# Kernel optimization log

Hardware: AMD Instinct MI355X
Metric: run time of the kernel (lower is better)

The kernel has to match this reference:

```python
import jax, jax.numpy as jnp
import numpy as np

EPS = 1e-5
BN_SCALE = 1.0 / np.sqrt(1.0 + EPS)  # inference BN with running_mean=0, running_var=1


def lrelu(x):
    return jnp.where(x >= 0, x, 0.2 * x)


def bn_affine(x, g, b, axis=1):
    shp = [1] * x.ndim
    shp[axis] = -1
    return x * (g.reshape(shp) * BN_SCALE) + b.reshape(shp)


def knn_idx(x, k):
    # x: (B, C, N) -> (B, N, k) indices of k nearest neighbors (incl. self)
    x2 = jnp.sum(x * x, axis=1)                       # (B, N)
    inner = jnp.einsum('bcn,bcm->bnm', x, x)          # (B, N, N)
    neg_dist = 2.0 * inner - x2[:, :, None] - x2[:, None, :]
    return jax.lax.top_k(neg_dist, k)[1]


def graph_feature(x, k):
    # x: (B, C, N) -> (B, 2C, N, k) edge features [x_j - x_i, x_i]
    B, C, N = x.shape
    idx = knn_idx(x, k)                               # (B, N, k)
    xt = jnp.transpose(x, (0, 2, 1))                  # (B, N, C)
    nbr = xt[jnp.arange(B)[:, None, None], idx]       # (B, N, k, C)
    ctr = xt[:, :, None, :]                           # (B, N, 1, C)
    feat = jnp.concatenate([nbr - ctr, jnp.broadcast_to(ctr, nbr.shape)], axis=-1)
    return jnp.transpose(feat, (0, 3, 1, 2))          # (B, 2C, N, k)


def edge_conv(x, W, g, b, k):
    # get_graph_feature -> 1x1 conv -> BN -> LeakyReLU -> max over neighbors
    f = graph_feature(x, k)
    h = jnp.einsum('oc,bcnk->bonk', W, f)
    return jnp.max(lrelu(bn_affine(h, g, b, axis=1)), axis=-1)  # (B, O, N)


def fps(xyz, m):
    # xyz: (B, 3, N) -> (B, m) farthest-point-sample indices, starting at index 0
    B, _, N = xyz.shape
    pts = jnp.transpose(xyz, (0, 2, 1))               # (B, N, 3)

    def body(carry, _):
        dists, last = carry
        p = jnp.take_along_axis(pts, last[:, None, None], axis=1)  # (B, 1, 3)
        d = jnp.sum((pts - p) ** 2, axis=-1)          # (B, N)
        dists = jnp.minimum(dists, d)
        nxt = jnp.argmax(dists, axis=-1).astype(jnp.int32)
        return (dists, nxt), last

    init = (jnp.full((B, N), 1e10, dtype=xyz.dtype), jnp.zeros((B,), jnp.int32))
    _, idxs = jax.lax.scan(body, init, None, length=m)
    return jnp.transpose(idxs, (1, 0))                # (B, m)


def gather_ch(x, idx):
    # x: (B, C, N), idx: (B, M) -> (B, C, M)
    B, C, _ = x.shape
    return jnp.take_along_axis(x, jnp.broadcast_to(idx[:, None, :], (B, C, idx.shape[1])), axis=2)


def aggregate(xyz, node, features, k):
    # xyz: (B,3,N), node: (B,3,M), features: (B,C,N) -> (B,C,M)
    B = xyz.shape[0]
    x2 = jnp.sum(xyz * xyz, axis=1)                   # (B, N)
    n2 = jnp.sum(node * node, axis=1)                 # (B, M)
    inner = jnp.einsum('bcm,bcn->bmn', node, xyz)     # (B, M, N)
    neg_d = 2.0 * inner - n2[:, :, None] - x2[:, None, :]
    idx = jax.lax.top_k(neg_d, k)[1]                  # (B, M, k) nearest points per node
    ft = jnp.transpose(features, (0, 2, 1))           # (B, N, C)
    grp = ft[jnp.arange(B)[:, None, None], idx]       # (B, M, k, C)
    return jnp.transpose(jnp.max(grp, axis=2), (0, 2, 1))  # (B, C, M)


def setup_inputs() -> dict:
    key = jax.random.key(0)
    ks = jax.random.split(key, 32)
    B, N, K, E = 8, 2048, 20, 1024

    def w(k_, o, c):
        return jax.random.normal(k_, (o, c), jnp.float32) / np.sqrt(c)

    def gb(k_, c):
        k1, k2 = jax.random.split(k_)
        return (jax.random.uniform(k1, (c,), jnp.float32, 0.5, 1.5),
                0.1 * jax.random.normal(k2, (c,), jnp.float32))

    g1, b1 = gb(ks[1], 64); g2, b2 = gb(ks[2], 64); g2m, b2m = gb(ks[3], E)
    g3, b3 = gb(ks[4], 256); g4, b4 = gb(ks[5], 256); g5, b5 = gb(ks[6], E)
    g6, b6 = gb(ks[7], 512); g7, b7 = gb(ks[8], 256)
    return {
        'x': jax.random.normal(ks[0], (B, 3, N), jnp.float32),
        'W1': w(ks[10], 64, 6), 'g1': g1, 'b1': b1,
        'W2': w(ks[11], 64, 128), 'g2': g2, 'b2': b2,
        'W2m': w(ks[12], E, 128), 'g2m': g2m, 'b2m': b2m,
        'W3': w(ks[13], 256, 512), 'g3': g3, 'b3': b3,
        'W4': w(ks[14], 256, 512), 'g4': g4, 'b4': b4,
        'W5': w(ks[15], E, 512), 'g5': g5, 'b5': b5,
        'Wl1': w(ks[16], 512, 2 * E), 'g6': g6, 'b6': b6,
        'Wl2': w(ks[17], 256, 512), 'bl2': 0.01 * jax.random.normal(ks[18], (256,), jnp.float32),
        'g7': g7, 'b7': b7,
        'Wl3': w(ks[19], 40, 256), 'bl3': 0.01 * jax.random.normal(ks[20], (40,), jnp.float32),
    }


def reference(x, W1, g1, b1, W2, g2, b2, W2m, g2m, b2m, W3, g3, b3,
              W4, g4, b4, W5, g5, b5, Wl1, g6, b6, Wl2, bl2, g7, b7, Wl3, bl3):
    K = 20
    B, _, N = x.shape
    xyz = x

    x1 = edge_conv(x, W1, g1, b1, K)                  # (B, 64, N)
    x2 = edge_conv(x1, W2, g2, b2, K)                 # (B, 64, N)
    xt1_ = jnp.concatenate([x1, x2], axis=1)          # (B, 128, N)
    xt1 = lrelu(bn_affine(jnp.einsum('oc,bcn->bon', W2m, xt1_), g2m, b2m, axis=1))

    idx = fps(xyz, N // 4)                            # (B, N/4)
    node1 = gather_ch(xyz, idx)                       # (B, 3, N/4)
    nf1 = gather_ch(xt1_, idx)                        # (B, 128, N/4)
    agg = aggregate(xyz, node1, xt1_, K)              # (B, 128, N/4)
    xm = jnp.concatenate([nf1, agg], axis=1)          # (B, 256, N/4)

    x3 = edge_conv(xm, W3, g3, b3, K // 2)            # (B, 256, N/4)
    x4 = edge_conv(x3, W4, g4, b4, K // 2)            # (B, 256, N/4)
    xt2 = lrelu(bn_affine(jnp.einsum('oc,bcn->bon', W5, jnp.concatenate([x3, x4], axis=1)), g5, b5, axis=1))

    v = jnp.concatenate([jnp.max(xt1, axis=-1), jnp.max(xt2, axis=-1)], axis=1)  # (B, 2E)
    h = lrelu(bn_affine(v @ Wl1.T, g6, b6, axis=1))   # dropout = identity (eval)
    h = lrelu(bn_affine(h @ Wl2.T + bl2, g7, b7, axis=1))
    logits = h @ Wl3.T + bl3                          # (B, 40)
    return (logits, node1)
```

## Files before the change

### kernel.cpp

```cpp
#include <hip/hip_runtime.h>

#define BN_SCALE 0.9999950000374997f

template <int CTRL>
__device__ __forceinline__ float dpp_fmax_step(float v) {
  int xi = __builtin_bit_cast(int, v);
  int ti = __builtin_amdgcn_update_dpp(xi, xi, CTRL, 0xf, 0xf, false);
  return fmaxf(v, __builtin_bit_cast(float, ti));
}
template <int CTRL>
__device__ __forceinline__ int dpp_imin_step(int v) {
  int t = __builtin_amdgcn_update_dpp(v, v, CTRL, 0xf, 0xf, false);
  return (t < v) ? t : v;
}
template <int CTRL>
__device__ __forceinline__ float dpp_fadd_step(float v) {
  int ti = __builtin_amdgcn_update_dpp(0, __builtin_bit_cast(int, v), CTRL, 0xf, 0xf, true);
  return v + __builtin_bit_cast(float, ti);
}
__device__ __forceinline__ float wave_fmax(float v) {
  v = dpp_fmax_step<0x111>(v);
  v = dpp_fmax_step<0x112>(v);
  v = dpp_fmax_step<0x114>(v);
  v = dpp_fmax_step<0x118>(v);
  v = dpp_fmax_step<0x142>(v);
  v = dpp_fmax_step<0x143>(v);
  return __builtin_bit_cast(float, __builtin_amdgcn_readlane(__builtin_bit_cast(int, v), 63));
}
__device__ __forceinline__ int wave_imin(int v) {
  v = dpp_imin_step<0x111>(v);
  v = dpp_imin_step<0x112>(v);
  v = dpp_imin_step<0x114>(v);
  v = dpp_imin_step<0x118>(v);
  v = dpp_imin_step<0x142>(v);
  v = dpp_imin_step<0x143>(v);
  return __builtin_amdgcn_readlane(v, 63);
}
__device__ __forceinline__ float wave_fadd(float v) {
  v = dpp_fadd_step<0x111>(v);
  v = dpp_fadd_step<0x112>(v);
  v = dpp_fadd_step<0x114>(v);
  v = dpp_fadd_step<0x118>(v);
  v = dpp_fadd_step<0x142>(v);
  v = dpp_fadd_step<0x143>(v);
  return __builtin_bit_cast(float, __builtin_amdgcn_readlane(__builtin_bit_cast(int, v), 63));
}

template <int R, bool SQPRE>
__device__ __forceinline__ void knn4_body(const float* __restrict__ Q, int qStrideB,
                                          const float* __restrict__ Xc, int cStrideB,
                                          int C, int M, int N, int k, int* __restrict__ idxOut,
                                          const float* __restrict__ sqPre,
                                          int b, int q0, char* smem) {
  constexpr int NR = 4 * R;
  float (*negd)[R * 256] = (float (*)[R * 256])smem;
  int tid = threadIdx.x;
  const float* qb = Q + (long)b * qStrideB + q0;
  const float* cb = Xc + (long)b * cStrideB;
  if constexpr (R % 4 == 0) {
    constexpr int H = R / 4;
    float d0[R], d1[R], d2[R], d3[R], sq[R];
    #pragma unroll
    for (int i = 0; i < R; ++i) { d0[i] = d1[i] = d2[i] = d3[i] = sq[i] = 0.f; }
    for (int c = 0; c < C; ++c) {
      float4 q4 = *(const float4*)(qb + (long)c * M);
      const float4* pc4 = (const float4*)(cb + (long)c * N);
      #pragma unroll
      for (int h = 0; h < H; ++h) {
        float4 xv = pc4[tid + 256 * h];
        if (!SQPRE) {
          sq[4 * h + 0] = fmaf(xv.x, xv.x, sq[4 * h + 0]);
          sq[4 * h + 1] = fmaf(xv.y, xv.y, sq[4 * h + 1]);
          sq[4 * h + 2] = fmaf(xv.z, xv.z, sq[4 * h + 2]);
          sq[4 * h + 3] = fmaf(xv.w, xv.w, sq[4 * h + 3]);
        }
        d0[4 * h + 0] = fmaf(q4.x, xv.x, d0[4 * h + 0]);
        d0[4 * h + 1] = fmaf(q4.x, xv.y, d0[4 * h + 1]);
        d0[4 * h + 2] = fmaf(q4.x, xv.z, d0[4 * h + 2]);
        d0[4 * h + 3] = fmaf(q4.x, xv.w, d0[4 * h + 3]);
        d1[4 * h + 0] = fmaf(q4.y, xv.x, d1[4 * h + 0]);
        d1[4 * h + 1] = fmaf(q4.y, xv.y, d1[4 * h + 1]);
        d1[4 * h + 2] = fmaf(q4.y, xv.z, d1[4 * h + 2]);
        d1[4 * h + 3] = fmaf(q4.y, xv.w, d1[4 * h + 3]);
        d2[4 * h + 0] = fmaf(q4.z, xv.x, d2[4 * h + 0]);
        d2[4 * h + 1] = fmaf(q4.z, xv.y, d2[4 * h + 1]);
        d2[4 * h + 2] = fmaf(q4.z, xv.z, d2[4 * h + 2]);
        d2[4 * h + 3] = fmaf(q4.z, xv.w, d2[4 * h + 3]);
        d3[4 * h + 0] = fmaf(q4.w, xv.x, d3[4 * h + 0]);
        d3[4 * h + 1] = fmaf(q4.w, xv.y, d3[4 * h + 1]);
        d3[4 * h + 2] = fmaf(q4.w, xv.z, d3[4 * h + 2]);
        d3[4 * h + 3] = fmaf(q4.w, xv.w, d3[4 * h + 3]);
      }
    }
    #pragma unroll
    for (int h = 0; h < H; ++h) {
      float4 s4;
      if (SQPRE) {
        s4 = ((const float4*)(sqPre + (long)b * N))[tid + 256 * h];
      } else {
        s4 = make_float4(sq[4 * h], sq[4 * h + 1], sq[4 * h + 2], sq[4 * h + 3]);
      }
      ((float4*)negd[0])[tid + 256 * h] =
          make_float4(2.f * d0[4 * h] - s4.x, 2.f * d0[4 * h + 1] - s4.y,
                      2.f * d0[4 * h + 2] - s4.z, 2.f * d0[4 * h + 3] - s4.w);
      ((float4*)negd[1])[tid + 256 * h] =
          make_float4(2.f * d1[4 * h] - s4.x, 2.f * d1[4 * h + 1] - s4.y,
                      2.f * d1[4 * h + 2] - s4.z, 2.f * d1[4 * h + 3] - s4.w);
      ((float4*)negd[2])[tid + 256 * h] =
          make_float4(2.f * d2[4 * h] - s4.x, 2.f * d2[4 * h + 1] - s4.y,
                      2.f * d2[4 * h + 2] - s4.z, 2.f * d2[4 * h + 3] - s4.w);
      ((float4*)negd[3])[tid + 256 * h] =
          make_float4(2.f * d3[4 * h] - s4.x, 2.f * d3[4 * h + 1] - s4.y,
                      2.f * d3[4 * h + 2] - s4.z, 2.f * d3[4 * h + 3] - s4.w);
    }
  } else {
    float d0[R], d1[R], d2[R], d3[R], sq[R];
    #pragma unroll
    for (int i = 0; i < R; ++i) { d0[i] = d1[i] = d2[i] = d3[i] = sq[i] = 0.f; }
    for (int c = 0; c < C; ++c) {
      float4 q4 = *(const float4*)(qb + (long)c * M);
      const float* pc = cb + (long)c * N;
      #pragma unroll
      for (int i = 0; i < R; ++i) {
        float xv = pc[tid + 256 * i];
        sq[i] = fmaf(xv, xv, sq[i]);
        d0[i] = fmaf(q4.x, xv, d0[i]);
        d1[i] = fmaf(q4.y, xv, d1[i]);
        d2[i] = fmaf(q4.z, xv, d2[i]);
        d3[i] = fmaf(q4.w, xv, d3[i]);
      }
    }
    #pragma unroll
    for (int i = 0; i < R; ++i) {
      int m = tid + 256 * i;
      negd[0][m] = 2.f * d0[i] - sq[i];
      negd[1][m] = 2.f * d1[i] - sq[i];
      negd[2][m] = 2.f * d2[i] - sq[i];
      negd[3][m] = 2.f * d3[i] - sq[i];
    }
  }
  __syncthreads();
  int lane = tid & 63, w = tid >> 6;
  const float* row = negd[w];
  int* outp = idxOut + ((long)b * M + (q0 + w)) * k;
  float v[NR];
  #pragma unroll
  for (int i = 0; i < NR; ++i) v[i] = row[lane + 64 * i];
  constexpr int G = NR / 4;
  for (int kk = 0; kk < k; ++kk) {
    float bv[G]; int br[G];
    #pragma unroll
    for (int g = 0; g < G; ++g) {
      float v0 = v[4 * g]; int r0 = 4 * g;
      #pragma unroll
      for (int j = 1; j < 4; ++j) {
        bool c = v[4 * g + j] > v0;
        v0 = c ? v[4 * g + j] : v0;
        r0 = c ? (4 * g + j) : r0;
      }
      bv[g] = v0; br[g] = r0;
    }
    #pragma unroll
    for (int s = G >> 1; s >= 1; s >>= 1) {
      #pragma unroll
      for (int i = 0; i < s; ++i) {
        bool c = bv[2 * i] >= bv[2 * i + 1];
        bv[i] = c ? bv[2 * i] : bv[2 * i + 1];
        br[i] = c ? br[2 * i] : br[2 * i + 1];
      }
    }
    float best = bv[0]; int ib = br[0];
    int bi = (best > -INFINITY) ? (lane + (ib << 6)) : N;
    float gmax = wave_fmax(best);
    int cand = (best == gmax) ? bi : 0x7FFFFFFF;
    int big = wave_imin(cand);
    if (lane == 0) outp[kk] = big;
    int ri = big >> 6;
    bool mine = (lane == (big & 63));
    #pragma unroll
    for (int i = 0; i < NR; ++i)
      if (i == ri) v[i] = mine ? -INFINITY : v[i];
  }
}

template <int R>
__global__ void knn4_kernel(const float* __restrict__ Q, int qStrideB,
                            const float* __restrict__ Xc, int cStrideB,
                            int C, int M, int N, int k, int* __restrict__ idxOut) {
  __shared__ __align__(16) char smem[R * 256 * 4 * 4];
  knn4_body<R, false>(Q, qStrideB, Xc, cStrideB, C, M, N, k, idxOut, nullptr,
                      blockIdx.y, blockIdx.x * 4, smem);
}

__device__ __forceinline__ void gemmPS_body(const float* __restrict__ X, int xStrideB, int C, int Np,
                                            const float* __restrict__ W, int ldw, int O,
                                            float* __restrict__ PtT, float* __restrict__ StT,
                                            int b, int n0, int o0, char* smem) {
  float (*Wp)[68] = (float (*)[68])smem;
  float (*Ws)[68] = (float (*)[68])(smem + 4352);
  float (*Xt)[68] = (float (*)[68])(smem + 8704);
  int tid = threadIdx.x;
  int to = tid % 16, tn = tid / 16;
  float accP[4][4] = {}, accS[4][4] = {};
  for (int c0 = 0; c0 < C; c0 += 16) {
    for (int e = tid; e < 16 * 64; e += 256) {
      int oo = e / 16, kk = e % 16;
      int c = c0 + kk, o = o0 + oo;
      bool ok = (c < C && o < O);
      Wp[kk][oo] = ok ? W[(long)o * ldw + c] : 0.f;
      Ws[kk][oo] = ok ? W[(long)o * ldw + C + c] : 0.f;
    }
    for (int e = tid; e < 16 * 64; e += 256) {
      int kk = e / 64, nn = e % 64;
      int c = c0 + kk, n = n0 + nn;
      Xt[kk][nn] = (c < C && n < Np) ? X[(long)b * xStrideB + (long)c * Np + n] : 0.f;
    }
    __syncthreads();
    for (int kk = 0; kk < 16; ++kk) {
      float4 xv = *(const float4*)&Xt[kk][tn * 4];
      float4 wp = *(const float4*)&Wp[kk][to * 4];
      float4 ws = *(const float4*)&Ws[kk][to * 4];
      float xs[4] = {xv.x, xv.y, xv.z, xv.w};
      float wps[4] = {wp.x, wp.y, wp.z, wp.w};
      float wss[4] = {ws.x, ws.y, ws.z, ws.w};
      #pragma unroll
      for (int i = 0; i < 4; ++i)
        #pragma unroll
        for (int j = 0; j < 4; ++j) {
          accP[i][j] = fmaf(xs[i], wps[j], accP[i][j]);
          accS[i][j] = fmaf(xs[i], wss[j], accS[i][j]);
        }
    }
    __syncthreads();
  }
  #pragma unroll
  for (int i = 0; i < 4; ++i) {
    int n = n0 + tn * 4 + i;
    if (n >= Np) continue;
    int o = o0 + to * 4;
    if (o + 3 < O) {
      long off = ((long)b * Np + n) * O + o;
      *(float4*)&PtT[off] = make_float4(accP[i][0], accP[i][1], accP[i][2], accP[i][3]);
      *(float4*)&StT[off] = make_float4(accS[i][0], accS[i][1], accS[i][2], accS[i][3]);
    } else {
      for (int j = 0; j < 4; ++j) {
        int oo = o + j;
        if (oo < O) {
          long off = ((long)b * Np + n) * O + oo;
          PtT[off] = accP[i][j];
          StT[off] = accS[i][j];
        }
      }
    }
  }
}

__device__ __forceinline__ void ecfinish_body64(const float* __restrict__ Pt, const float* __restrict__ St,
                                                const int* __restrict__ idx, int k, int O, int Np,
                                                const float* __restrict__ g, const float* __restrict__ bb,
                                                float* __restrict__ outp, long oStrideB,
                                                float* __restrict__ sqOut,
                                                int b, int blk) {
  int tid = threadIdx.x;
  int o = tid & 63;
  int n = blk * 4 + (tid >> 6);
  const float* PtB = Pt + (long)b * Np * O;
  const float* StB = St + (long)b * Np * O;
  const int* ip = idx + ((long)b * Np + n) * k;
  float mx = -INFINITY, mn = INFINITY;
  for (int kk = 0; kk < k; ++kk) {
    float v = PtB[(long)ip[kk] * O + o];
    mx = fmaxf(mx, v); mn = fminf(mn, v);
  }
  float ctrP = PtB[(long)n * O + o];
  float ctrS = StB[(long)n * O + o];
  float gs = g[o] * BN_SCALE;
  float m = (gs >= 0.f) ? mx : mn;
  float h = (ctrS - ctrP + m) * gs + bb[o];
  float out = h >= 0.f ? h : 0.2f * h;
  outp[(long)b * oStrideB + (long)o * Np + n] = out;
  if (sqOut) {
    int obits = __builtin_bit_cast(int, out);
    float acc = 0.f;
    #pragma unroll
    for (int c = 0; c < 64; ++c) {
      float hv = __builtin_bit_cast(float, __builtin_amdgcn_readlane(obits, c));
      acc = fmaf(hv, hv, acc);
    }
    if (o == 0) sqOut[(long)b * Np + n] = acc;
  }
}

__global__ void ecfinish_kernel(const float* __restrict__ Pt, const float* __restrict__ St,
                                const int* __restrict__ idx, int k, int O, int Np,
                                const float* __restrict__ g, const float* __restrict__ bb,
                                float* __restrict__ outp, long oStrideB) {
  int b = blockIdx.y;
  int n = blockIdx.x * blockDim.y + threadIdx.y;
  int o = threadIdx.x;
  const float* PtB = Pt + (long)b * Np * O;
  const float* StB = St + (long)b * Np * O;
  const int* ip = idx + ((long)b * Np + n) * k;
  float mx = -INFINITY, mn = INFINITY;
  for (int kk = 0; kk < k; ++kk) {
    float v = PtB[(long)ip[kk] * O + o];
    mx = fmaxf(mx, v); mn = fminf(mn, v);
  }
  float ctrP = PtB[(long)n * O + o];
  float ctrS = StB[(long)n * O + o];
  float gs = g[o] * BN_SCALE;
  float m = (gs >= 0.f) ? mx : mn;
  float h = (ctrS - ctrP + m) * gs + bb[o];
  outp[(long)b * oStrideB + (long)o * Np + n] = h >= 0.f ? h : 0.2f * h;
}

__device__ __forceinline__ void gemm_colmax_body(const float* __restrict__ X, int xStrideB, int C, int Np,
                                                 const float* __restrict__ W, int ldw, int O,
                                                 const float* __restrict__ g, const float* __restrict__ bb,
                                                 float* __restrict__ partial,
                                                 int b, int n0, int o0, int nt, int nNT, char* smem) {
  float (*Wt)[68] = (float (*)[68])smem;
  float (*Xt)[68] = (float (*)[68])(smem + 4352);
  int tid = threadIdx.x;
  int to = tid % 16, tn = tid / 16;
  float acc[4][4] = {};
  for (int c0 = 0; c0 < C; c0 += 16) {
    for (int e = tid; e < 16 * 64; e += 256) {
      int oo = e / 16, kk = e % 16;
      int c = c0 + kk, o = o0 + oo;
      Wt[kk][oo] = (c < C && o < O) ? W[(long)o * ldw + c] : 0.f;
    }
    for (int e = tid; e < 16 * 64; e += 256) {
      int kk = e / 64, nn = e % 64;
      int c = c0 + kk, n = n0 + nn;
      Xt[kk][nn] = (c < C && n < Np) ? X[(long)b * xStrideB + (long)c * Np + n] : 0.f;
    }
    __syncthreads();
    for (int kk = 0; kk < 16; ++kk) {
      float4 xv = *(const float4*)&Xt[kk][tn * 4];
      float4 wv = *(const float4*)&Wt[kk][to * 4];
      float xs[4] = {xv.x, xv.y, xv.z, xv.w};
      float wvs[4] = {wv.x, wv.y, wv.z, wv.w};
      #pragma unroll
      for (int i = 0; i < 4; ++i)
        #pragma unroll
        for (int j = 0; j < 4; ++j) acc[i][j] = fmaf(xs[i], wvs[j], acc[i][j]);
    }
    __syncthreads();
  }
  float vm[4];
  #pragma unroll
  for (int j = 0; j < 4; ++j) {
    int o = o0 + to * 4 + j;
    float gs = g[o] * BN_SCALE, bo = bb[o];
    float m = -INFINITY;
    #pragma unroll
    for (int i = 0; i < 4; ++i) {
      float h = acc[i][j] * gs + bo;
      h = h >= 0.f ? h : 0.2f * h;
      m = fmaxf(m, h);
    }
    vm[j] = m;
  }
  #pragma unroll
  for (int j = 0; j < 4; ++j) Xt[tn][to * 4 + j] = vm[j];
  __syncthreads();
  for (int s = 8; s > 0; s >>= 1) {
    if (tn < s)
      for (int j = 0; j < 4; ++j)
        Xt[tn][to * 4 + j] = fmaxf(Xt[tn][to * 4 + j], Xt[tn + s][to * 4 + j]);
    __syncthreads();
  }
  if (tn == 0)
    for (int j = 0; j < 4; ++j) {
      int o = o0 + to * 4 + j;
      partial[((long)b * nNT + nt) * O + o] = Xt[0][to * 4 + j];
    }
}

__global__ void gemm_colmax_kernel(const float* __restrict__ X, int xStrideB, int C, int Np,
                                   const float* __restrict__ W, int ldw, int O,
                                   const float* __restrict__ g, const float* __restrict__ bb,
                                   float* __restrict__ partial) {
  __shared__ __align__(16) char smem[8704];
  gemm_colmax_body(X, xStrideB, C, Np, W, ldw, O, g, bb, partial,
                   blockIdx.z, blockIdx.x * 64, blockIdx.y * 64, blockIdx.x, gridDim.x, smem);
}

__device__ __forceinline__ void xmfill_body(const float* __restrict__ xt1, int N,
                                            const int* __restrict__ fpsI,
                                            const int* __restrict__ idxA, int k, int M,
                                            float* __restrict__ xm, int xe) {
  long t = (long)xe * 256 + threadIdx.x;
  int i = (int)(t % M);
  int c = (int)((t / M) % 128);
  int b = (int)(t / ((long)128 * M));
  const float* xb = xt1 + (long)b * 128 * N + (long)c * N;
  float* xmB = xm + (long)b * 256 * M;
  xmB[(long)c * M + i] = xb[fpsI[(long)b * M + i]];
  const int* ip = idxA + ((long)b * M + i) * k;
  float best = -INFINITY;
  for (int kk = 0; kk < k; ++kk) best = fmaxf(best, xb[ip[kk]]);
  xmB[(long)(128 + c) * M + i] = best;
}

template <int FIRST, int LAST>
__device__ __forceinline__ void fps_body_rg(const float* __restrict__ xyz, int N, int M,
                                            int it0, int it1,
                                            int* __restrict__ fpsIdx, float* __restrict__ node1,
                                            float* __restrict__ distSv, int* __restrict__ lastSv,
                                            int b, char* smem) {
  #pragma clang fp contract(off)
  float4* sp4 = (float4*)smem;
  int*    fidx = (int*)(smem + 32768);
  float4* wvc  = (float4*)(smem + 32768 + 2048);
  int*    wis  = (int*)(smem + 32768 + 2048 + 128);
  int tid = threadIdx.x;
  int lane = tid & 63, w = tid >> 6;
  const float* xb = xyz + (long)b * 3 * N;
  for (int n = tid; n < N; n += 256) {
    sp4[((n & 7) << 8) | (n >> 3)] = make_float4(xb[n], xb[N + n], xb[2 * N + n], 0.f);
  }
  if (!FIRST) {
    for (int e = tid; e < it0; e += 256) fidx[e] = fpsIdx[(long)b * M + e];
  }
  __syncthreads();
  float4 pt[8];
  #pragma unroll
  for (int i = 0; i < 8; ++i) pt[i] = sp4[(i << 8) | tid];
  float dist[8];
  int last;
  float lx, ly, lz;
  if (FIRST) {
    #pragma unroll
    for (int i = 0; i < 8; ++i) dist[i] = 1e10f;
    last = 0;
    float4 l0 = sp4[0];
    lx = l0.x; ly = l0.y; lz = l0.z;
  } else {
    #pragma unroll
    for (int i = 0; i < 8; ++i) dist[i] = distSv[(long)b * 2048 + i * 256 + tid];
    last = lastSv[b];
    float4 lp = sp4[((last & 7) << 8) | (last >> 3)];
    lx = lp.x; ly = lp.y; lz = lp.z;
  }
  int base = tid * 8;
  for (int it = it0; it < it1; ++it) {
    int p = it & 1;
    if (tid == 0) fidx[it] = last;
    float best = -INFINITY; int bi = N;
    #pragma unroll
    for (int i = 0; i < 8; ++i) {
      float dx = pt[i].x - lx, dy = pt[i].y - ly, dz = pt[i].z - lz;
      float dx2 = dx * dx, dy2 = dy * dy, dz2 = dz * dz;
      float d = (dx2 + dy2) + dz2;
      float dn = dist[i];
      if (d < dn) dn = d;
      dist[i] = dn;
      if (dn > best) { best = dn; bi = base + i; }
    }
    float cx = pt[0].x, cy = pt[0].y, cz = pt[0].z;
    #pragma unroll
    for (int i = 1; i < 8; ++i) {
      bool c = (bi == base + i);
      cx = c ? pt[i].x : cx; cy = c ? pt[i].y : cy; cz = c ? pt[i].z : cz;
    }
    float gmax = wave_fmax(best);
    int cand = (best == gmax) ? bi : 0x7FFFFFFF;
    int wbi = wave_imin(cand);
    if (bi == wbi) { wvc[p * 4 + w] = make_float4(gmax, cx, cy, cz); wis[p * 4 + w] = wbi; }
    __syncthreads();
    float4 c0 = wvc[p * 4 + 0], c1 = wvc[p * 4 + 1], c2 = wvc[p * 4 + 2], c3 = wvc[p * 4 + 3];
    int i0 = wis[p * 4 + 0], i1 = wis[p * 4 + 1], i2 = wis[p * 4 + 2], i3 = wis[p * 4 + 3];
    float bv = c0.x; int bbi = i0; lx = c0.y; ly = c0.z; lz = c0.w;
    { bool c = (c1.x > bv) || (c1.x == bv && i1 < bbi);
      bv = c ? c1.x : bv; bbi = c ? i1 : bbi; lx = c ? c1.y : lx; ly = c ? c1.z : ly; lz = c ? c1.w : lz; }
    { bool c = (c2.x > bv) || (c2.x == bv && i2 < bbi);
      bv = c ? c2.x : bv; bbi = c ? i2 : bbi; lx = c ? c2.y : lx; ly = c ? c2.z : ly; lz = c ? c2.w : lz; }
    { bool c = (c3.x > bv) || (c3.x == bv && i3 < bbi);
      bv = c ? c3.x : bv; bbi = c ? i3 : bbi; lx = c ? c3.y : lx; ly = c ? c3.z : ly; lz = c ? c3.w : lz; }
    last = bbi;
  }
  if (!LAST) {
    for (int e = tid; e < it1; e += 256) {
      if (e >= it0) fpsIdx[(long)b * M + e] = fidx[e];
    }
    #pragma unroll
    for (int i = 0; i < 8; ++i) distSv[(long)b * 2048 + i * 256 + tid] = dist[i];
    if (tid == 0) lastSv[b] = last;
  } else {
    for (int e = tid; e < M; e += 256) fpsIdx[(long)b * M + e] = fidx[e];
    for (int e = tid; e < 3 * M; e += 256) {
      int c = e / M, i = e % M;
      int src = fidx[i];
      float4 ptc = sp4[((src & 7) << 8) | (src >> 3)];
      node1[(long)b * 3 * M + e] = (c == 0) ? ptc.x : (c == 1) ? ptc.y : ptc.z;
    }
  }
}

template <int FIRST, int LAST, bool SQP>
__global__ void knnfpsgemm_kernel(const float* __restrict__ Q, int qStrideB,
                                  const float* __restrict__ Xc, int cStrideB,
                                  int C, int Mq, int N, int k, int* __restrict__ idxOut,
                                  const float* __restrict__ W, int ldw, int O,
                                  float* __restrict__ Pt, float* __restrict__ St,
                                  const float* __restrict__ xyz, int Mf, int it0, int it1,
                                  int* __restrict__ fpsIdx, float* __restrict__ node1,
                                  float* __restrict__ distSv, int* __restrict__ lastSv,
                                  const float* __restrict__ sqPre,
                                  int nQblk, int nGblk, int nB) {
  __shared__ __align__(16) char smem[32768 + 2048 + 128 + 32];
  int bid = blockIdx.x;
  if (bid < nB) {
    __builtin_amdgcn_s_setprio(1);
    fps_body_rg<FIRST, LAST>(xyz, N, Mf, it0, it1, fpsIdx, node1, distSv, lastSv, bid, smem);
    __builtin_amdgcn_s_setprio(0);
  } else if (bid < nB + nB * nQblk) {
    int e = bid - nB;
    knn4_body<8, SQP>(Q, qStrideB, Xc, cStrideB, C, Mq, N, k, idxOut, sqPre,
                      e / nQblk, (e % nQblk) * 4, smem);
  } else {
    int e = bid - nB - nB * nQblk;
    gemmPS_body(Xc, cStrideB, C, N, W, ldw, O, Pt, St,
                e / nGblk, (e % nGblk) * 64, 0, smem);
  }
}

__global__ void ecfps_kernel(const float* __restrict__ Pt, const float* __restrict__ St,
                             const int* __restrict__ idx, int k, int O, int Np,
                             const float* __restrict__ g, const float* __restrict__ bb,
                             float* __restrict__ outp, long oStrideB,
                             float* __restrict__ sqOut,
                             const float* __restrict__ xyz, int N, int Mf, int it0, int it1,
                             int* __restrict__ fpsIdx, float* __restrict__ node1,
                             float* __restrict__ distSv, int* __restrict__ lastSv,
                             int nEperB, int nB) {
  __shared__ __align__(16) char smem[32768 + 2048 + 128 + 32];
  int bid = blockIdx.x;
  if (bid < nB) {
    __builtin_amdgcn_s_setprio(1);
    fps_body_rg<0, 0>(xyz, N, Mf, it0, it1, fpsIdx, node1, distSv, lastSv, bid, smem);
    __builtin_amdgcn_s_setprio(0);
  } else {
    int e = bid - nB;
    ecfinish_body64(Pt, St, idx, k, O, Np, g, bb, outp, oStrideB, sqOut,
                    e / nEperB, e % nEperB);
  }
}

__global__ void ecfagg_kernel(const float* __restrict__ Pt, const float* __restrict__ St,
                              const int* __restrict__ idxS2, int k2, int O2, int Np2,
                              const float* __restrict__ g2, const float* __restrict__ b2,
                              float* __restrict__ out2, long oStrideB2,
                              const float* __restrict__ Qn, int qStrideB,
                              const float* __restrict__ Xc, int cStrideB,
                              int Cq, int Mq, int Nc, int kq, int* __restrict__ idxAgg,
                              int nQblk, int nEperB) {
  __shared__ __align__(16) char smem[32768];
  int bid = blockIdx.x;
  if (bid % 5 == 0) {
    int a = bid / 5;
    knn4_body<8, false>(Qn, qStrideB, Xc, cStrideB, Cq, Mq, Nc, kq, idxAgg, nullptr,
                        a / nQblk, (a % nQblk) * 4, smem);
  } else {
    int e = bid - bid / 5 - 1;
    ecfinish_body64(Pt, St, idxS2, k2, O2, Np2, g2, b2, out2, oStrideB2, nullptr,
                    e / nEperB, e % nEperB);
  }
}

__global__ void colmaxxm_kernel(const float* __restrict__ X, int xStrideB, int C, int Np,
                                const float* __restrict__ W, int ldw, int O,
                                const float* __restrict__ g, const float* __restrict__ bb,
                                float* __restrict__ partial, int nNT, int nOT,
                                const float* __restrict__ xt1, int N,
                                const int* __restrict__ fpsI, const int* __restrict__ idxA,
                                int kq, int M, float* __restrict__ xm) {
  __shared__ __align__(16) char smem[8704];
  int bid = blockIdx.x;
  if (bid % 3 == 0) {
    xmfill_body(xt1, N, fpsI, idxA, kq, M, xm, bid / 3);
  } else {
    int e = bid - bid / 3 - 1;
    int per = nNT * nOT;
    int b = e / per, r = e % per;
    int nt = r % nNT, ot = r / nNT;
    gemm_colmax_body(X, xStrideB, C, Np, W, ldw, O, g, bb, partial,
                     b, nt * 64, ot * 64, nt, nNT, smem);
  }
}

__global__ void knngemm_kernel(const float* __restrict__ Xin, int xStrideB,
                               int C, int Mq, int N, int k, int* __restrict__ idxOut,
                               const float* __restrict__ W, int ldw, int O,
                               float* __restrict__ Pt, float* __restrict__ St,
                               int nQblk, int nGn, int nGo, int nB) {
  __shared__ __align__(16) char smem[13056];
  int bid = blockIdx.x;
  if (bid < nB * nQblk) {
    knn4_body<2, false>(Xin, xStrideB, Xin, xStrideB, C, Mq, N, k, idxOut, nullptr,
                        bid / nQblk, (bid % nQblk) * 4, smem);
  } else {
    int e = bid - nB * nQblk;
    int per = nGn * nGo;
    int b = e / per, r = e % per;
    int nt = r % nGn, ot = r / nGn;
    gemmPS_body(Xin, xStrideB, C, N, W, ldw, O, Pt, St, b, nt * 64, ot * 64, smem);
  }
}

__global__ void head_kernel(const float* __restrict__ partA, int NTa,
                            const float* __restrict__ partB, int NTb,
                            const float* __restrict__ Wl1, const float* __restrict__ g6, const float* __restrict__ b6,
                            const float* __restrict__ Wl2, const float* __restrict__ bl2,
                            const float* __restrict__ g7, const float* __restrict__ b7,
                            const float* __restrict__ Wl3, const float* __restrict__ bl3,
                            float* __restrict__ logits) {
  __shared__ float v[2048];
  __shared__ float h1[512];
  __shared__ float h2[256];
  int b = blockIdx.x, tid = threadIdx.x;
  int lane = tid & 63, w = tid >> 6;
  for (int o = tid; o < 1024; o += 256) {
    float m = -INFINITY;
    for (int t = 0; t < NTa; ++t) m = fmaxf(m, partA[((long)b * NTa + t) * 1024 + o]);
    v[o] = m;
    float m2 = -INFINITY;
    for (int t = 0; t < NTb; ++t) m2 = fmaxf(m2, partB[((long)b * NTb + t) * 1024 + o]);
    v[1024 + o] = m2;
  }
  __syncthreads();
  for (int o = w; o < 512; o += 4) {
    const float4* wr = (const float4*)(Wl1 + (long)o * 2048);
    const float4* vp = (const float4*)v;
    float s = 0.f;
    #pragma unroll
    for (int j = 0; j < 8; ++j) {
      float4 w4 = wr[lane + 64 * j];
      float4 v4 = vp[lane + 64 * j];
      s = fmaf(w4.x, v4.x, s); s = fmaf(w4.y, v4.y, s);
      s = fmaf(w4.z, v4.z, s); s = fmaf(w4.w, v4.w, s);
    }
    float t = wave_fadd(s);
    if (lane == 0) {
      float h = t * (g6[o] * BN_SCALE) + b6[o];
      h1[o] = h >= 0.f ? h : 0.2f * h;
    }
  }
  __syncthreads();
  for (int o = w; o < 256; o += 4) {
    const float4* wr = (const float4*)(Wl2 + (long)o * 512);
    const float4* hp = (const float4*)h1;
    float s = 0.f;
    #pragma unroll
    for (int j = 0; j < 2; ++j) {
      float4 w4 = wr[lane + 64 * j];
      float4 v4 = hp[lane + 64 * j];
      s = fmaf(w4.x, v4.x, s); s = fmaf(w4.y, v4.y, s);
      s = fmaf(w4.z, v4.z, s); s = fmaf(w4.w, v4.w, s);
    }
    float t = wave_fadd(s);
    if (lane == 0) {
      float sb = t + bl2[o];
      float h = sb * (g7[o] * BN_SCALE) + b7[o];
      h2[o] = h >= 0.f ? h : 0.2f * h;
    }
  }
  __syncthreads();
  for (int o = w; o < 40; o += 4) {
    const float4* wr = (const float4*)(Wl3 + (long)o * 256);
    const float4* hp = (const float4*)h2;
    float4 w4 = wr[lane];
    float4 v4 = hp[lane];
    float s = fmaf(w4.x, v4.x, 0.f);
    s = fmaf(w4.y, v4.y, s); s = fmaf(w4.z, v4.z, s); s = fmaf(w4.w, v4.w, s);
    float t = wave_fadd(s);
    if (lane == 0) logits[(long)b * 40 + o] = t + bl3[o];
  }
}

extern "C" void kernel_launch(void* const* d_in, const int* in_sizes, int n_in,
                              void* d_out, int out_size, void* d_ws, size_t ws_size,
                              hipStream_t stream) {
  const float* x   = (const float*)d_in[0];
  const float* W1  = (const float*)d_in[1];
  const float* g1  = (const float*)d_in[2];
  const float* b1  = (const float*)d_in[3];
  const float* W2  = (const float*)d_in[4];
  const float* g2  = (const float*)d_in[5];
  const float* b2  = (const float*)d_in[6];
  const float* W2m = (const float*)d_in[7];
  const float* g2m = (const float*)d_in[8];
  const float* b2m = (const float*)d_in[9];
  const float* W3  = (const float*)d_in[10];
  const float* g3  = (const float*)d_in[11];
  const float* b3  = (const float*)d_in[12];
  const float* W4  = (const float*)d_in[13];
  const float* g4  = (const float*)d_in[14];
  const float* b4  = (const float*)d_in[15];
  const float* W5  = (const float*)d_in[16];
  const float* g5  = (const float*)d_in[17];
  const float* b5  = (const float*)d_in[18];
  const float* Wl1 = (const float*)d_in[19];
  const float* g6  = (const float*)d_in[20];
  const float* b6  = (const float*)d_in[21];
  const float* Wl2 = (const float*)d_in[22];
  const float* bl2 = (const float*)d_in[23];
  const float* g7  = (const float*)d_in[24];
  const float* b7  = (const float*)d_in[25];
  const float* Wl3 = (const float*)d_in[26];
  const float* bl3 = (const float*)d_in[27];
  float* outF = (float*)d_out;

  const int B = 8, N = 2048, K = 20, M = 512, K2 = 10;

  float* ws    = (float*)d_ws;
  float* xt1   = ws;
  float* xm    = xt1 + (size_t)B * 128 * N;
  float* xc    = xm  + (size_t)B * 256 * M;
  float* Pt    = xc  + (size_t)B * 512 * M;
  float* St    = Pt  + (size_t)B * N * 64;
  float* partA = St  + (size_t)B * N * 64;
  float* partB = partA + (size_t)B * 32 * 1024;
  int*   idxK  = (int*)(partB + (size_t)B * 8 * 1024);
  int*   fpsI  = idxK + (size_t)B * N * K;
  float* fpsDist = (float*)(fpsI + (size_t)B * M);
  int*   fpsLast = (int*)(fpsDist + (size_t)B * 2048);
  int*   idxAgg  = fpsLast + 64;
  float* sqS2    = (float*)(idxAgg + (size_t)B * M * K);

  float* logits = outF;
  float* node1  = outF + 320;

  dim3 t256(256);
  const int nQblk = N / 4;
  const int nGblk = N / 64;
  const int nFused = B + B * nQblk + B * nGblk;
  const int nQa = M / 4;
  const int IT1 = 208, IT2 = 304;

  knnfpsgemm_kernel<1, 0, false><<<dim3(nFused), t256, 0, stream>>>(
      x, 3 * N, x, 3 * N, 3, N, N, K, idxK,
      W1, 6, 64, Pt, St,
      x, M, 0, IT1, fpsI, node1, fpsDist, fpsLast, nullptr, nQblk, nGblk, B);

  ecfps_kernel<<<dim3(B + B * (N / 4)), t256, 0, stream>>>(
      Pt, St, idxK, K, 64, N, g1, b1, xt1, (long)128 * N, sqS2,
      x, N, M, IT1, IT2, fpsI, node1, fpsDist, fpsLast, N / 4, B);

  knnfpsgemm_kernel<0, 1, true><<<dim3(nFused), t256, 0, stream>>>(
      xt1, 128 * N, xt1, 128 * N, 64, N, N, K, idxK,
      W2, 128, 64, Pt, St,
      x, M, IT2, M, fpsI, node1, fpsDist, fpsLast, sqS2, nQblk, nGblk, B);

  ecfagg_kernel<<<dim3(B * nQa + B * (N / 4)), t256, 0, stream>>>(
      Pt, St, idxK, K, 64, N, g2, b2, xt1 + (size_t)64 * N, (long)128 * N,
      node1, 3 * M, x, 3 * N, 3, M, N, K, idxAgg, nQa, N / 4);

  colmaxxm_kernel<<<dim3((B * 128 * M) / 256 + B * 32 * 16), t256, 0, stream>>>(
      xt1, 128 * N, 128, N, W2m, 128, 1024, g2m, b2m, partA, 32, 16,
      xt1, N, fpsI, idxAgg, K, M, xm);

  knngemm_kernel<<<dim3(B * nQa + B * (M / 64) * (256 / 64)), t256, 0, stream>>>(
      xm, 256 * M, 256, M, M, K2, idxK, W3, 512, 256, Pt, St, nQa, M / 64, 256 / 64, B);
  ecfinish_kernel<<<dim3(M, B), dim3(256, 1), 0, stream>>>(Pt, St, idxK, K2, 256, M, g3, b3, xc, (long)512 * M);

  knngemm_kernel<<<dim3(B * nQa + B * (M / 64) * (256 / 64)), t256, 0, stream>>>(
      xc, 512 * M, 256, M, M, K2, idxK, W4, 512, 256, Pt, St, nQa, M / 64, 256 / 64, B);
  ecfinish_kernel<<<dim3(M, B), dim3(256, 1), 0, stream>>>(Pt, St, idxK, K2, 256, M, g4, b4,
                                                           xc + (size_t)256 * M, (long)512 * M);

  gemm_colmax_kernel<<<dim3(M / 64, 1024 / 64, B), t256, 0, stream>>>(xc, 512 * M, 512, M, W5, 512, 1024,
                                                                      g5, b5, partB);

  head_kernel<<<dim3(B), t256, 0, stream>>>(partA, N / 64, partB, M / 64,
                                            Wl1, g6, b6, Wl2, bl2, g7, b7, Wl3, bl3, logits);
}
```

Measured before the change: 1.064 ms.

## Cache per-group maxima in knn top-k and split FPS points into SoA

The top-k selection in the knn body now keeps the per-group maxima of four values across iterations. After each pick it recomputes only the group that lost an element, instead of rescanning every value each round, which cuts the ALU work per selected neighbor. The FPS body stores point coordinates as three separate float arrays instead of padded float4. This shrinks shared memory so the fused kernels declare smaller LDS allocations, which may raise occupancy. The dynamic group recompute adds predicated branches over all groups, and the register layout changes.

```diff
diff --git a/kernel.cpp b/kernel.cpp
--- a/kernel.cpp
+++ b/kernel.cpp
@@ -147,29 +147,32 @@
   #pragma unroll
   for (int i = 0; i < NR; ++i) v[i] = row[lane + 64 * i];
   constexpr int G = NR / 4;
+  float bv[G]; int br[G];
+  #pragma unroll
+  for (int g = 0; g < G; ++g) {
+    float v0 = v[4 * g]; int r0 = 4 * g;
+    #pragma unroll
+    for (int j = 1; j < 4; ++j) {
+      bool c = v[4 * g + j] > v0;
+      v0 = c ? v[4 * g + j] : v0;
+      r0 = c ? (4 * g + j) : r0;
+    }
+    bv[g] = v0; br[g] = r0;
+  }
   for (int kk = 0; kk < k; ++kk) {
-    float bv[G]; int br[G];
-    #pragma unroll
-    for (int g = 0; g < G; ++g) {
-      float v0 = v[4 * g]; int r0 = 4 * g;
-      #pragma unroll
-      for (int j = 1; j < 4; ++j) {
-        bool c = v[4 * g + j] > v0;
-        v0 = c ? v[4 * g + j] : v0;
-        r0 = c ? (4 * g + j) : r0;
-      }
-      bv[g] = v0; br[g] = r0;
-    }
+    float mv[G]; int mi[G];
+    #pragma unroll
+    for (int g = 0; g < G; ++g) { mv[g] = bv[g]; mi[g] = br[g]; }
     #pragma unroll
     for (int s = G >> 1; s >= 1; s >>= 1) {
       #pragma unroll
       for (int i = 0; i < s; ++i) {
-        bool c = bv[2 * i] >= bv[2 * i + 1];
-        bv[i] = c ? bv[2 * i] : bv[2 * i + 1];
-        br[i] = c ? br[2 * i] : br[2 * i + 1];
+        bool c = mv[2 * i] >= mv[2 * i + 1];
+        mv[i] = c ? mv[2 * i] : mv[2 * i + 1];
+        mi[i] = c ? mi[2 * i] : mi[2 * i + 1];
       }
     }
-    float best = bv[0]; int ib = br[0];
+    float best = mv[0]; int ib = mi[0];
     int bi = (best > -INFINITY) ? (lane + (ib << 6)) : N;
     float gmax = wave_fmax(best);
     int cand = (best == gmax) ? bi : 0x7FFFFFFF;
@@ -180,6 +183,20 @@
     #pragma unroll
     for (int i = 0; i < NR; ++i)
       if (i == ri) v[i] = mine ? -INFINITY : v[i];
+    int gi = ri >> 2;
+    #pragma unroll
+    for (int g = 0; g < G; ++g) {
+      if (g == gi) {
+        float v0 = v[4 * g]; int r0 = 4 * g;
+        #pragma unroll
+        for (int j = 1; j < 4; ++j) {
+          bool c = v[4 * g + j] > v0;
+          v0 = c ? v[4 * g + j] : v0;
+          r0 = c ? (4 * g + j) : r0;
+        }
+        bv[g] = v0; br[g] = r0;
+      }
+    }
   }
 }
 
@@ -411,23 +428,29 @@
                                             float* __restrict__ distSv, int* __restrict__ lastSv,
                                             int b, char* smem) {
   #pragma clang fp contract(off)
-  float4* sp4 = (float4*)smem;
-  int*    fidx = (int*)(smem + 32768);
-  float4* wvc  = (float4*)(smem + 32768 + 2048);
-  int*    wis  = (int*)(smem + 32768 + 2048 + 128);
+  float* px = (float*)smem;
+  float* py = (float*)(smem + 8192);
+  float* pz = (float*)(smem + 16384);
+  int*   fidx = (int*)(smem + 24576);
+  float4* wvc = (float4*)(smem + 26624);
+  int*   wis  = (int*)(smem + 26752);
   int tid = threadIdx.x;
   int lane = tid & 63, w = tid >> 6;
   const float* xb = xyz + (long)b * 3 * N;
   for (int n = tid; n < N; n += 256) {
-    sp4[((n & 7) << 8) | (n >> 3)] = make_float4(xb[n], xb[N + n], xb[2 * N + n], 0.f);
+    int s = ((n & 7) << 8) | (n >> 3);
+    px[s] = xb[n]; py[s] = xb[N + n]; pz[s] = xb[2 * N + n];
   }
   if (!FIRST) {
     for (int e = tid; e < it0; e += 256) fidx[e] = fpsIdx[(long)b * M + e];
   }
   __syncthreads();
-  float4 pt[8];
+  float ptx[8], pty[8], ptz[8];
   #pragma unroll
-  for (int i = 0; i < 8; ++i) pt[i] = sp4[(i << 8) | tid];
+  for (int i = 0; i < 8; ++i) {
+    int s = (i << 8) | tid;
+    ptx[i] = px[s]; pty[i] = py[s]; ptz[i] = pz[s];
+  }
   float dist[8];
   int last;
   float lx, ly, lz;
@@ -435,14 +458,14 @@
     #pragma unroll
     for (int i = 0; i < 8; ++i) dist[i] = 1e10f;
     last = 0;
-    float4 l0 = sp4[0];
-    lx = l0.x; ly = l0.y; lz = l0.z;
+    int s0 = 0;
+    lx = px[s0]; ly = py[s0]; lz = pz[s0];
   } else {
     #pragma unroll
     for (int i = 0; i < 8; ++i) dist[i] = distSv[(long)b * 2048 + i * 256 + tid];
     last = lastSv[b];
-    float4 lp = sp4[((last & 7) << 8) | (last >> 3)];
-    lx = lp.x; ly = lp.y; lz = lp.z;
+    int sl = ((last & 7) << 8) | (last >> 3);
+    lx = px[sl]; ly = py[sl]; lz = pz[sl];
   }
   int base = tid * 8;
   for (int it = it0; it < it1; ++it) {
@@ -451,7 +474,7 @@
     float best = -INFINITY; int bi = N;
     #pragma unroll
     for (int i = 0; i < 8; ++i) {
-      float dx = pt[i].x - lx, dy = pt[i].y - ly, dz = pt[i].z - lz;
+      float dx = ptx[i] - lx, dy = pty[i] - ly, dz = ptz[i] - lz;
       float dx2 = dx * dx, dy2 = dy * dy, dz2 = dz * dz;
       float d = (dx2 + dy2) + dz2;
       float dn = dist[i];
@@ -459,11 +482,11 @@
       dist[i] = dn;
       if (dn > best) { best = dn; bi = base + i; }
     }
-    float cx = pt[0].x, cy = pt[0].y, cz = pt[0].z;
+    float cx = ptx[0], cy = pty[0], cz = ptz[0];
     #pragma unroll
     for (int i = 1; i < 8; ++i) {
       bool c = (bi == base + i);
-      cx = c ? pt[i].x : cx; cy = c ? pt[i].y : cy; cz = c ? pt[i].z : cz;
+      cx = c ? ptx[i] : cx; cy = c ? pty[i] : cy; cz = c ? ptz[i] : cz;
     }
     float gmax = wave_fmax(best);
     int cand = (best == gmax) ? bi : 0x7FFFFFFF;
@@ -493,8 +516,8 @@
     for (int e = tid; e < 3 * M; e += 256) {
       int c = e / M, i = e % M;
       int src = fidx[i];
-      float4 ptc = sp4[((src & 7) << 8) | (src >> 3)];
-      node1[(long)b * 3 * M + e] = (c == 0) ? ptc.x : (c == 1) ? ptc.y : ptc.z;
+      int s = ((src & 7) << 8) | (src >> 3);
+      node1[(long)b * 3 * M + e] = (c == 0) ? px[s] : (c == 1) ? py[s] : pz[s];
     }
   }
 }
@@ -510,7 +533,7 @@
                                   float* __restrict__ distSv, int* __restrict__ lastSv,
                                   const float* __restrict__ sqPre,
                                   int nQblk, int nGblk, int nB) {
-  __shared__ __align__(16) char smem[32768 + 2048 + 128 + 32];
+  __shared__ __align__(16) char smem[32768];
   int bid = blockIdx.x;
   if (bid < nB) {
     __builtin_amdgcn_s_setprio(1);
@@ -536,7 +559,7 @@
                              int* __restrict__ fpsIdx, float* __restrict__ node1,
                              float* __restrict__ distSv, int* __restrict__ lastSv,
                              int nEperB, int nB) {
-  __shared__ __align__(16) char smem[32768 + 2048 + 128 + 32];
+  __shared__ __align__(16) char smem[26784];
   int bid = blockIdx.x;
   if (bid < nB) {
     __builtin_amdgcn_s_setprio(1);
```

Measured after the change: 1.057 ms. About the same (-0.7%).
